# Kernel tuning notes

Measured on AMD Instinct MI355X. Metric: run time of the kernel, lower is better.

Reference implementation:

```python
import jax, jax.numpy as jnp
import numpy as np

TOP_K = 2


def setup_inputs() -> dict:
    key = jax.random.key(0)
    k1, k2 = jax.random.split(key)
    hidden_states = jax.random.normal(k1, (32768, 2048), dtype=jnp.float32)
    weight = jax.random.normal(k2, (64, 2048), dtype=jnp.float32) * 0.02
    return {"hidden_states": hidden_states, "weight": weight}


def reference(hidden_states, weight):
    # logits = hidden_states @ weight.T : [tokens, num_experts]
    logits = jnp.einsum("td,ed->te", hidden_states, weight)
    # softmax in float32 (matches torch dtype=torch.float)
    probs = jax.nn.softmax(logits.astype(jnp.float32), axis=-1)
    topk_prob, topk_idx = jax.lax.top_k(probs, TOP_K)  # descending, like torch.topk
    topk_prob = topk_prob / jnp.sum(topk_prob, axis=-1, keepdims=True)
    return logits, topk_prob.astype(logits.dtype), topk_idx
```

## Files before the change

kernel.cpp:

```cpp
#include <hip/hip_runtime.h>

#define T_TOKENS 32768
#define DIM      2048
#define NEXP     64
#define KC       64
#define NCHUNK   (DIM / KC)
#define TPB      256
#define TOK_BLK  64
#define LSTR     65

__global__ __launch_bounds__(TPB, 2) void router_kernel(
    const float* __restrict__ hs, const float* __restrict__ w,
    float* __restrict__ logits, float* __restrict__ tkp, float* __restrict__ tki)
{
    __shared__ float lds[2][KC * LSTR];

    const int tid  = threadIdx.x;
    const int lane = tid & 63;
    const int wv   = __builtin_amdgcn_readfirstlane(tid >> 6);
    const int ebase = wv * 16;
    const int t0   = blockIdx.x * TOK_BLK;

    float acc[16];
#pragma unroll
    for (int i = 0; i < 16; ++i) acc[i] = 0.f;

    float4 st[4];

#pragma unroll
    for (int i = 0; i < 4; ++i) {
        int f = i * TPB + tid, row = f >> 4, c4 = f & 15;
        st[i] = *(const float4*)(hs + (size_t)(t0 + row) * DIM + c4 * 4);
    }
#pragma unroll
    for (int i = 0; i < 4; ++i) {
        int f = i * TPB + tid, row = f >> 4, c4 = f & 15;
        lds[0][(c4 * 4 + 0) * LSTR + row] = st[i].x;
        lds[0][(c4 * 4 + 1) * LSTR + row] = st[i].y;
        lds[0][(c4 * 4 + 2) * LSTR + row] = st[i].z;
        lds[0][(c4 * 4 + 3) * LSTR + row] = st[i].w;
    }
    __syncthreads();

#pragma unroll 1
    for (int kc = 0; kc < NCHUNK; ++kc) {
        const int buf = kc & 1;

        if (kc + 1 < NCHUNK) {
#pragma unroll
            for (int i = 0; i < 4; ++i) {
                int f = i * TPB + tid, row = f >> 4, c4 = f & 15;
                st[i] = *(const float4*)(hs + (size_t)(t0 + row) * DIM +
                                         (kc + 1) * KC + c4 * 4);
            }
        }

        const float* wbase = w + (size_t)ebase * DIM + kc * KC;
#pragma unroll
        for (int k4 = 0; k4 < 16; ++k4) {
            float h0 = lds[buf][(k4 * 4 + 0) * LSTR + lane];
            float h1 = lds[buf][(k4 * 4 + 1) * LSTR + lane];
            float h2 = lds[buf][(k4 * 4 + 2) * LSTR + lane];
            float h3 = lds[buf][(k4 * 4 + 3) * LSTR + lane];
#pragma unroll
            for (int e = 0; e < 16; ++e) {
                const float* wr = wbase + e * DIM + k4 * 4;
                acc[e] = fmaf(h0, wr[0], acc[e]);
                acc[e] = fmaf(h1, wr[1], acc[e]);
                acc[e] = fmaf(h2, wr[2], acc[e]);
                acc[e] = fmaf(h3, wr[3], acc[e]);
            }
        }

        if (kc + 1 < NCHUNK) {
#pragma unroll
            for (int i = 0; i < 4; ++i) {
                int f = i * TPB + tid, row = f >> 4, c4 = f & 15;
                lds[buf ^ 1][(c4 * 4 + 0) * LSTR + row] = st[i].x;
                lds[buf ^ 1][(c4 * 4 + 1) * LSTR + row] = st[i].y;
                lds[buf ^ 1][(c4 * 4 + 2) * LSTR + row] = st[i].z;
                lds[buf ^ 1][(c4 * 4 + 3) * LSTR + row] = st[i].w;
            }
        }
        __syncthreads();
    }

    float* ltile = &lds[0][0];
#pragma unroll
    for (int i = 0; i < 4; ++i) {
        *(float4*)(logits + (size_t)(t0 + lane) * NEXP + ebase + i * 4) =
            make_float4(acc[i * 4 + 0], acc[i * 4 + 1], acc[i * 4 + 2], acc[i * 4 + 3]);
    }
#pragma unroll
    for (int i = 0; i < 16; ++i)
        ltile[lane * LSTR + ebase + i] = acc[i];
    __syncthreads();

    if (tid < TOK_BLK) {
        const int t = tid;
        float m1 = -1e30f; int i1 = 0;
#pragma unroll
        for (int e = 0; e < NEXP; ++e) {
            float v = ltile[t * LSTR + e];
            if (v > m1) { m1 = v; i1 = e; }
        }
        float m2 = -1e30f; int i2 = 0;
#pragma unroll
        for (int e = 0; e < NEXP; ++e) {
            float v = ltile[t * LSTR + e];
            if (e != i1 && v > m2) { m2 = v; i2 = e; }
        }
        float e2v = __expf(m2 - m1);
        float s = 1.f + e2v;
        tkp[(size_t)(t0 + t) * 2 + 0] = 1.f / s;
        tkp[(size_t)(t0 + t) * 2 + 1] = e2v / s;
        tki[(size_t)(t0 + t) * 2 + 0] = (float)i1;
        tki[(size_t)(t0 + t) * 2 + 1] = (float)i2;
    }
}

extern "C" void kernel_launch(void* const* d_in, const int* in_sizes, int n_in,
                              void* d_out, int out_size, void* d_ws, size_t ws_size,
                              hipStream_t stream) {
    const float* hs = (const float*)d_in[0];
    const float* w  = (const float*)d_in[1];
    float* logits = (float*)d_out;
    float* tkp    = logits + (size_t)T_TOKENS * NEXP;
    float* tki    = tkp + (size_t)T_TOKENS * 2;

    dim3 grid(T_TOKENS / TOK_BLK);
    router_kernel<<<grid, TPB, 0, stream>>>(hs, w, logits, tkp, tki);
}
```

Before: 1.131 ms.

## Stage weights in LDS and compute two tokens per thread with larger blocks

Router GEMM now stages each K-chunk of the weight matrix in shared memory alongside the transposed hidden-state tile, instead of every wave reading weights straight from global memory. Blocks grow to 512 threads covering 128 tokens. Each thread accumulates 2 tokens × 8 experts, reading float2 hidden values and float4 weight vectors from LDS. This aims to cut redundant global/L2 weight traffic and raise FMA-to-load ratio, at the cost of more LDS usage, a smaller K-chunk (more barriers), and possible LDS bank conflicts on the broadcast weight reads.

```diff
diff --git a/kernel.cpp b/kernel.cpp
--- a/kernel.cpp
+++ b/kernel.cpp
@@ -1,113 +1,129 @@
 #include <hip/hip_runtime.h>
 
 #define T_TOKENS 32768
-#define DIM      2048
+#define DIMK     2048
 #define NEXP     64
-#define KC       64
-#define NCHUNK   (DIM / KC)
-#define TPB      256
-#define TOK_BLK  64
-#define LSTR     65
+#define KC       32
+#define NCHUNK   (DIMK / KC)
+#define TPB      512
+#define TOKB     128
+#define EPW      8
+#define HSTR     130
+#define WSTR     32
+#define HBUF     (KC * HSTR)
+#define WBUF     (NEXP * WSTR)
+#define BUFSZ    (HBUF + WBUF)
+#define LTSTR    68
 
-__global__ __launch_bounds__(TPB, 2) void router_kernel(
-    const float* __restrict__ hs, const float* __restrict__ w,
+__global__ __launch_bounds__(TPB) void router_kernel(
+    const float* __restrict__ hs, const float* __restrict__ wt,
     float* __restrict__ logits, float* __restrict__ tkp, float* __restrict__ tki)
 {
-    __shared__ float lds[2][KC * LSTR];
+    __shared__ float smem[2 * BUFSZ];
 
     const int tid  = threadIdx.x;
     const int lane = tid & 63;
-    const int wv   = __builtin_amdgcn_readfirstlane(tid >> 6);
-    const int ebase = wv * 16;
-    const int t0   = blockIdx.x * TOK_BLK;
+    const int wv   = tid >> 6;
+    const int ebase = wv * EPW;
+    const int t0   = blockIdx.x * TOKB;
 
-    float acc[16];
+    float acc0[EPW], acc1[EPW];
 #pragma unroll
-    for (int i = 0; i < 16; ++i) acc[i] = 0.f;
+    for (int i = 0; i < EPW; ++i) { acc0[i] = 0.f; acc1[i] = 0.f; }
 
-    float4 st[4];
+    const int htok0 = tid >> 3,          hk40 = tid & 7;
+    const int htok1 = (512 + tid) >> 3,  hk41 = tid & 7;
+    const int we0   = tid >> 3,          wk40 = tid & 7;
 
-#pragma unroll
-    for (int i = 0; i < 4; ++i) {
-        int f = i * TPB + tid, row = f >> 4, c4 = f & 15;
-        st[i] = *(const float4*)(hs + (size_t)(t0 + row) * DIM + c4 * 4);
-    }
-#pragma unroll
-    for (int i = 0; i < 4; ++i) {
-        int f = i * TPB + tid, row = f >> 4, c4 = f & 15;
-        lds[0][(c4 * 4 + 0) * LSTR + row] = st[i].x;
-        lds[0][(c4 * 4 + 1) * LSTR + row] = st[i].y;
-        lds[0][(c4 * 4 + 2) * LSTR + row] = st[i].z;
-        lds[0][(c4 * 4 + 3) * LSTR + row] = st[i].w;
+    float4 ph0, ph1, pw0;
+
+    ph0 = *(const float4*)(hs + (size_t)(t0 + htok0) * DIMK + hk40 * 4);
+    ph1 = *(const float4*)(hs + (size_t)(t0 + htok1) * DIMK + hk41 * 4);
+    pw0 = *(const float4*)(wt + (size_t)we0 * DIMK + wk40 * 4);
+    {
+        float* bh = smem;
+        float* bw = smem + HBUF;
+        bh[(hk40*4+0)*HSTR + htok0] = ph0.x; bh[(hk40*4+1)*HSTR + htok0] = ph0.y;
+        bh[(hk40*4+2)*HSTR + htok0] = ph0.z; bh[(hk40*4+3)*HSTR + htok0] = ph0.w;
+        bh[(hk41*4+0)*HSTR + htok1] = ph1.x; bh[(hk41*4+1)*HSTR + htok1] = ph1.y;
+        bh[(hk41*4+2)*HSTR + htok1] = ph1.z; bh[(hk41*4+3)*HSTR + htok1] = ph1.w;
+        *(float4*)&bw[we0*WSTR + wk40*4] = pw0;
     }
     __syncthreads();
 
 #pragma unroll 1
     for (int kc = 0; kc < NCHUNK; ++kc) {
         const int buf = kc & 1;
+        const float* bh = smem + buf * BUFSZ;
+        const float* bw = bh + HBUF;
 
         if (kc + 1 < NCHUNK) {
-#pragma unroll
-            for (int i = 0; i < 4; ++i) {
-                int f = i * TPB + tid, row = f >> 4, c4 = f & 15;
-                st[i] = *(const float4*)(hs + (size_t)(t0 + row) * DIM +
-                                         (kc + 1) * KC + c4 * 4);
-            }
+            const int kb = (kc + 1) * KC;
+            ph0 = *(const float4*)(hs + (size_t)(t0 + htok0) * DIMK + kb + hk40 * 4);
+            ph1 = *(const float4*)(hs + (size_t)(t0 + htok1) * DIMK + kb + hk41 * 4);
+            pw0 = *(const float4*)(wt + (size_t)we0 * DIMK + kb + wk40 * 4);
         }
 
-        const float* wbase = w + (size_t)ebase * DIM + kc * KC;
 #pragma unroll
-        for (int k4 = 0; k4 < 16; ++k4) {
-            float h0 = lds[buf][(k4 * 4 + 0) * LSTR + lane];
-            float h1 = lds[buf][(k4 * 4 + 1) * LSTR + lane];
-            float h2 = lds[buf][(k4 * 4 + 2) * LSTR + lane];
-            float h3 = lds[buf][(k4 * 4 + 3) * LSTR + lane];
+        for (int k4 = 0; k4 < 8; ++k4) {
+            float2 h0 = *(const float2*)&bh[(k4*4+0)*HSTR + 2*lane];
+            float2 h1 = *(const float2*)&bh[(k4*4+1)*HSTR + 2*lane];
+            float2 h2 = *(const float2*)&bh[(k4*4+2)*HSTR + 2*lane];
+            float2 h3 = *(const float2*)&bh[(k4*4+3)*HSTR + 2*lane];
 #pragma unroll
-            for (int e = 0; e < 16; ++e) {
-                const float* wr = wbase + e * DIM + k4 * 4;
-                acc[e] = fmaf(h0, wr[0], acc[e]);
-                acc[e] = fmaf(h1, wr[1], acc[e]);
-                acc[e] = fmaf(h2, wr[2], acc[e]);
-                acc[e] = fmaf(h3, wr[3], acc[e]);
+            for (int e = 0; e < EPW; ++e) {
+                float4 w4 = *(const float4*)&bw[(ebase + e)*WSTR + k4*4];
+                acc0[e] = fmaf(h0.x, w4.x, acc0[e]);
+                acc0[e] = fmaf(h1.x, w4.y, acc0[e]);
+                acc0[e] = fmaf(h2.x, w4.z, acc0[e]);
+                acc0[e] = fmaf(h3.x, w4.w, acc0[e]);
+                acc1[e] = fmaf(h0.y, w4.x, acc1[e]);
+                acc1[e] = fmaf(h1.y, w4.y, acc1[e]);
+                acc1[e] = fmaf(h2.y, w4.z, acc1[e]);
+                acc1[e] = fmaf(h3.y, w4.w, acc1[e]);
             }
         }
 
         if (kc + 1 < NCHUNK) {
-#pragma unroll
-            for (int i = 0; i < 4; ++i) {
-                int f = i * TPB + tid, row = f >> 4, c4 = f & 15;
-                lds[buf ^ 1][(c4 * 4 + 0) * LSTR + row] = st[i].x;
-                lds[buf ^ 1][(c4 * 4 + 1) * LSTR + row] = st[i].y;
-                lds[buf ^ 1][(c4 * 4 + 2) * LSTR + row] = st[i].z;
-                lds[buf ^ 1][(c4 * 4 + 3) * LSTR + row] = st[i].w;
-            }
+            float* nh = smem + (buf ^ 1) * BUFSZ;
+            float* nw = nh + HBUF;
+            nh[(hk40*4+0)*HSTR + htok0] = ph0.x; nh[(hk40*4+1)*HSTR + htok0] = ph0.y;
+            nh[(hk40*4+2)*HSTR + htok0] = ph0.z; nh[(hk40*4+3)*HSTR + htok0] = ph0.w;
+            nh[(hk41*4+0)*HSTR + htok1] = ph1.x; nh[(hk41*4+1)*HSTR + htok1] = ph1.y;
+            nh[(hk41*4+2)*HSTR + htok1] = ph1.z; nh[(hk41*4+3)*HSTR + htok1] = ph1.w;
+            *(float4*)&nw[we0*WSTR + wk40*4] = pw0;
         }
         __syncthreads();
     }
 
-    float* ltile = &lds[0][0];
+    float* tile = smem;
+    const int tA = 2*lane, tB = 2*lane + 1;
 #pragma unroll
-    for (int i = 0; i < 4; ++i) {
-        *(float4*)(logits + (size_t)(t0 + lane) * NEXP + ebase + i * 4) =
-            make_float4(acc[i * 4 + 0], acc[i * 4 + 1], acc[i * 4 + 2], acc[i * 4 + 3]);
+    for (int i = 0; i < 2; ++i) {
+        *(float4*)(logits + (size_t)(t0 + tA) * NEXP + ebase + i*4) =
+            make_float4(acc0[i*4+0], acc0[i*4+1], acc0[i*4+2], acc0[i*4+3]);
+        *(float4*)(logits + (size_t)(t0 + tB) * NEXP + ebase + i*4) =
+            make_float4(acc1[i*4+0], acc1[i*4+1], acc1[i*4+2], acc1[i*4+3]);
     }
 #pragma unroll
-    for (int i = 0; i < 16; ++i)
-        ltile[lane * LSTR + ebase + i] = acc[i];
+    for (int i = 0; i < EPW; ++i) {
+        tile[tA*LTSTR + ebase + i] = acc0[i];
+        tile[tB*LTSTR + ebase + i] = acc1[i];
+    }
     __syncthreads();
 
-    if (tid < TOK_BLK) {
+    if (tid < TOKB) {
         const int t = tid;
         float m1 = -1e30f; int i1 = 0;
 #pragma unroll
         for (int e = 0; e < NEXP; ++e) {
-            float v = ltile[t * LSTR + e];
+            float v = tile[t*LTSTR + e];
             if (v > m1) { m1 = v; i1 = e; }
         }
         float m2 = -1e30f; int i2 = 0;
 #pragma unroll
         for (int e = 0; e < NEXP; ++e) {
-            float v = ltile[t * LSTR + e];
+            float v = tile[t*LTSTR + e];
             if (e != i1 && v > m2) { m2 = v; i2 = e; }
         }
         float e2v = __expf(m2 - m1);
@@ -123,11 +139,11 @@
                               void* d_out, int out_size, void* d_ws, size_t ws_size,
                               hipStream_t stream) {
     const float* hs = (const float*)d_in[0];
-    const float* w  = (const float*)d_in[1];
+    const float* wt = (const float*)d_in[1];
     float* logits = (float*)d_out;
     float* tkp    = logits + (size_t)T_TOKENS * NEXP;
     float* tki    = tkp + (size_t)T_TOKENS * 2;
 
-    dim3 grid(T_TOKENS / TOK_BLK);
-    router_kernel<<<grid, TPB, 0, stream>>>(hs, w, logits, tkp, tki);
+    dim3 grid(T_TOKENS / TOKB);
+    router_kernel<<<grid, TPB, 0, stream>>>(hs, wt, logits, tkp, tki);
 }
```

After: 1.677 ms. 1.48x slower.
